# Optimization experiments

Hardware: AMD Instinct MI355X
Metric: run time of the kernel (lower is better)

Reference implementation:

```python
import jax, jax.numpy as jnp
import numpy as np
from functools import partial

B, S, H = 1, 2048, 1024
F, E, K = 2048, 8, 2


def setup_inputs() -> dict:
    key = jax.random.key(0)
    ks = jax.random.split(key, 7)
    x = jax.random.normal(ks[0], (B, S, H), dtype=jnp.float32)
    weights = jax.random.uniform(ks[1], (B * S, E), dtype=jnp.float32)
    top_weights = jax.random.uniform(ks[2], (B * S, K), dtype=jnp.float32)
    top_experts = jax.random.randint(ks[3], (B * S, K), 0, E).astype(jnp.int64)
    scale = 0.02  # keep activations in a sane range
    w1 = jax.random.normal(ks[4], (E, F, H), dtype=jnp.float32) * scale
    v1 = jax.random.normal(ks[5], (E, F, H), dtype=jnp.float32) * scale
    w2 = jax.random.normal(ks[6], (E, F, H), dtype=jnp.float32) * scale
    return {"x": x, "weights": weights, "top_weights": top_weights,
            "top_experts": top_experts, "w1": w1, "v1": v1, "w2": w2}


def _moe_forward(x, top_weights, top_experts, w1, v1, w2):
    b, s, h = x.shape
    xf = x.reshape(-1, h)  # [T, H]
    n_exp = w1.shape[0]
    # combine weight per (token, expert): sum over top-k slots routed to e
    onehot = jax.nn.one_hot(top_experts, n_exp, dtype=x.dtype)      # [T, K, E]
    cw = jnp.einsum('tk,tke->et', top_weights, onehot)              # [E, T]

    def body(acc, inputs):
        w1e, v1e, w2e, cwe = inputs  # [F,H], [F,H], [F,H], [T]
        gate = jax.nn.silu(xf @ w1e.T)       # [T, F]
        inter = gate * (xf @ v1e.T)          # GLU
        down = inter @ w2e                   # [T, H]
        return acc + cwe[:, None] * down, None

    out, _ = jax.lax.scan(body, jnp.zeros_like(xf), (w1, v1, w2, cw))
    return out.reshape(b, s, h)


def reference(x, weights, top_weights, top_experts, w1, v1, w2):
    # `weights` (full router probs) is accepted but unused, as in the original.
    return _moe_forward(x, top_weights, top_experts, w1, v1, w2)
```

## Files before the change

### kernel.cpp

```cpp
#include <hip/hip_runtime.h>
#include <hip/hip_bf16.h>


#define T_ 2048
#define H_ 1024
#define F_ 2048
#define E_ 8

#define SCAP 768
#define NSLOT (E_ * SCAP)
#define MAXT2 (NSLOT / 128)

typedef unsigned short u16;
typedef short s8v __attribute__((ext_vector_type(8)));
typedef float f4v __attribute__((ext_vector_type(4)));
typedef unsigned short u16x4 __attribute__((ext_vector_type(4)));

__device__ __forceinline__ u16 f2bf(float f) {
    union { float f; unsigned u; } v; v.f = f;
    unsigned r = v.u + 0x7FFF + ((v.u >> 16) & 1);
    return (u16)(r >> 16);
}
__device__ __forceinline__ unsigned pkbf(float a, float b) {
    __hip_bfloat162 h = __float22bfloat162_rn(make_float2(a, b));
    union { __hip_bfloat162 h; unsigned u; } c; c.h = h; return c.u;
}
__device__ __forceinline__ int4 cvt8(const float4 a, const float4 b) {
    int4 r; r.x = (int)pkbf(a.x, a.y); r.y = (int)pkbf(a.z, a.w);
    r.z = (int)pkbf(b.x, b.y); r.w = (int)pkbf(b.z, b.w); return r;
}
__device__ __forceinline__ void async16(void* lds, const void* g) {
    __builtin_amdgcn_global_load_lds(
        (const __attribute__((address_space(1))) unsigned*)g,
        (__attribute__((address_space(3))) unsigned*)lds, 16, 0, 0);
}

__global__ void router_kernel(const int* __restrict__ te, const float* __restrict__ tw,
                              int* __restrict__ slot_tok, float* __restrict__ slot_w,
                              int* __restrict__ tok_slot,
                              int* __restrict__ tile_e, int* __restrict__ tile_s,
                              int* __restrict__ ntiles) {
    __shared__ int cnt[E_];
    __shared__ int s_any;
    int tid = threadIdx.x;
    if (tid < E_) cnt[tid] = 0;
    if (tid == 0) s_any = 0;
    __syncthreads();
    int any = 0;
    for (int i = tid; i < 2 * T_; i += 256) if (i & 1) any |= te[i];
    if (any) atomicOr(&s_any, 1);
    __syncthreads();
    bool is32 = (s_any != 0);
    for (int t = tid; t < T_; t += 256) {
        int e0 = is32 ? te[2 * t]     : te[4 * t];
        int e1 = is32 ? te[2 * t + 1] : te[4 * t + 2];
        float w0 = tw[2 * t], w1 = tw[2 * t + 1];
        if (e0 == e1) {
            int p = atomicAdd(&cnt[e0], 1);
            int s = (p < SCAP) ? e0 * SCAP + p : -1;
            if (s >= 0) { slot_tok[s] = t; slot_w[s] = w0 + w1; }
            tok_slot[2 * t] = s; tok_slot[2 * t + 1] = -1;
        } else {
            int p = atomicAdd(&cnt[e0], 1);
            int s = (p < SCAP) ? e0 * SCAP + p : -1;
            if (s >= 0) { slot_tok[s] = t; slot_w[s] = w0; }
            tok_slot[2 * t] = s;
            p = atomicAdd(&cnt[e1], 1);
            s = (p < SCAP) ? e1 * SCAP + p : -1;
            if (s >= 0) { slot_tok[s] = t; slot_w[s] = w1; }
            tok_slot[2 * t + 1] = s;
        }
    }
    __syncthreads();
    for (int e = 0; e < E_; ++e) {
        int c = min(cnt[e], SCAP);
        int pc = min((c + 127) & ~127, SCAP);
        for (int p = c + tid; p < pc; p += 256) {
            slot_tok[e * SCAP + p] = -1; slot_w[e * SCAP + p] = 0.f;
        }
    }
    __syncthreads();
    if (tid == 0) {
        int nt = 0;
        for (int e = 0; e < E_; ++e) {
            int pc = min((min(cnt[e], SCAP) + 127) & ~127, SCAP);
            for (int s = 0; s < pc; s += 128) { tile_e[nt] = e; tile_s[nt] = e * SCAP + s; ++nt; }
        }
        *ntiles = nt;
    }
}

__global__ void tcvt8_kernel(const float* __restrict__ src0, u16* __restrict__ dst0) {
    const float* src = src0 + (size_t)blockIdx.z * F_ * H_;
    u16* dst = dst0 + (size_t)blockIdx.z * H_ * F_;
    __shared__ __align__(16) u16 tile[64][72];
    int bc = blockIdx.x * 64, br = blockIdx.y * 64;
    int tx = threadIdx.x, ty = threadIdx.y;
    for (int r = ty; r < 64; r += 32) {
        const float* p = src + (size_t)(br + r) * H_ + bc + tx * 8;
        float4 v0 = *(const float4*)p;
        float4 v1 = *(const float4*)(p + 4);
        u16* q = &tile[r][tx * 8];
        q[0] = f2bf(v0.x); q[1] = f2bf(v0.y); q[2] = f2bf(v0.z); q[3] = f2bf(v0.w);
        q[4] = f2bf(v1.x); q[5] = f2bf(v1.y); q[6] = f2bf(v1.z); q[7] = f2bf(v1.w);
    }
    __syncthreads();
    for (int c = ty; c < 64; c += 32) {
        u16 tmp[8];
#pragma unroll
        for (int j = 0; j < 8; ++j) tmp[j] = tile[tx * 8 + j][c];
        *(int4*)&dst[(size_t)(bc + c) * F_ + br + tx * 8] = *(int4*)tmp;
    }
}

__global__ void gather_x_kernel(const float* __restrict__ x, const int* __restrict__ slot_tok,
                                const int* __restrict__ tile_s, const int* __restrict__ ntiles,
                                u16* __restrict__ xg) {
    if ((int)blockIdx.x >= *ntiles) return;
    int base = tile_s[blockIdx.x];
    int tid = threadIdx.x;
    __shared__ int stok[128];
    if (tid < 128) stok[tid] = slot_tok[base + tid];
    __syncthreads();
    int c0 = blockIdx.y * 2048;
    for (int c = c0 + tid; c < c0 + 2048; c += 256) {
        int r = c >> 7, co = (c & 127) * 8;
        int tok = stok[r];
        u16* dst = xg + ((size_t)(base + r) << 10) + co;
        if (tok < 0) { *(int4*)dst = make_int4(0, 0, 0, 0); }
        else {
            const float* p = x + ((size_t)tok << 10) + co;
            *(int4*)dst = cvt8(*(const float4*)p, *(const float4*)(p + 4));
        }
    }
}

__global__ __launch_bounds__(256, 4) void glu_async_kernel(
        const u16* __restrict__ xg, const float* __restrict__ w1,
        const float* __restrict__ v1, const int* __restrict__ tile_e,
        const int* __restrict__ tile_s, const int* __restrict__ ntiles,
        const float* __restrict__ slot_w, u16* __restrict__ inter) {
    int bt = blockIdx.y;
    if (bt >= *ntiles) return;
    int e = tile_e[bt], s0 = tile_s[bt];
    int f0 = blockIdx.x * 64;
    __shared__ __align__(16) u16 As[2][128 * 32];
    __shared__ __align__(16) u16 B1s[2][64 * 32];
    __shared__ __align__(16) u16 B2s[2][64 * 32];
    __shared__ float swv[128];
    int tid = threadIdx.x;
    int lane = tid & 63, wave = tid >> 6;
    int wm = wave >> 1, wn = wave & 1;
    int ml = lane & 15, q = lane >> 4;
    if (tid < 128) swv[tid] = slot_w[s0 + tid];

    int row0 = (wave << 4) + (lane >> 2);
    int row1 = row0 + 64;
    int cs = ((lane & 3) ^ ((row0 >> 1) & 3)) << 3;
    const u16* gA0  = xg + ((size_t)(s0 + row0) << 10) + cs;
    const u16* gA1  = xg + ((size_t)(s0 + row1) << 10) + cs;
    int l0 = (row0 << 5) + ((lane & 3) << 3);
    int l1 = (row1 << 5) + ((lane & 3) << 3);

    int brow = tid >> 2;
    int bc   = tid & 3;
    const size_t wofs = (size_t)e * F_ * H_;
    const float* gB1 = w1 + wofs + (size_t)(f0 + brow) * H_ + bc * 8;
    const float* gB2 = v1 + wofs + (size_t)(f0 + brow) * H_ + bc * 8;
    int lb = (brow << 5) + ((bc ^ ((brow >> 1) & 3)) << 3);

    int xs = (q ^ ((lane >> 1) & 3)) << 3;

    f4v accg[4][2] = {};
    f4v accu[4][2] = {};

    float4 rb1a = *(const float4*)(gB1);
    float4 rb1b = *(const float4*)(gB1 + 4);
    float4 rb2a = *(const float4*)(gB2);
    float4 rb2b = *(const float4*)(gB2 + 4);
    async16(&As[0][l0], gA0);
    async16(&As[0][l1], gA1);

    const int NT = H_ / 32;
    int cur = 0;
    for (int t = 0; t < NT; ++t) {
        *(int4*)(&B1s[cur][lb]) = cvt8(rb1a, rb1b);
        *(int4*)(&B2s[cur][lb]) = cvt8(rb2a, rb2b);
        __syncthreads();
        if (t + 1 < NT) {
            int k = (t + 1) << 5;
            rb1a = *(const float4*)(gB1 + k);
            rb1b = *(const float4*)(gB1 + k + 4);
            rb2a = *(const float4*)(gB2 + k);
            rb2b = *(const float4*)(gB2 + k + 4);
            int nx = cur ^ 1;
            async16(&As[nx][l0], gA0 + k);
            async16(&As[nx][l1], gA1 + k);
        }
        s8v a[4], b1[2], b2[2];
#pragma unroll
        for (int i = 0; i < 4; ++i)
            a[i]  = *(const s8v*)(&As[cur][(wm * 64 + i * 16 + ml) * 32 + xs]);
#pragma unroll
        for (int j = 0; j < 2; ++j) {
            b1[j] = *(const s8v*)(&B1s[cur][(wn * 32 + j * 16 + ml) * 32 + xs]);
            b2[j] = *(const s8v*)(&B2s[cur][(wn * 32 + j * 16 + ml) * 32 + xs]);
        }
#pragma unroll
        for (int i = 0; i < 4; ++i)
#pragma unroll
            for (int j = 0; j < 2; ++j) {
                accg[i][j] = __builtin_amdgcn_mfma_f32_16x16x32_bf16(a[i], b1[j], accg[i][j], 0, 0, 0);
                accu[i][j] = __builtin_amdgcn_mfma_f32_16x16x32_bf16(a[i], b2[j], accu[i][j], 0, 0, 0);
            }
        cur ^= 1;
    }
#pragma unroll
    for (int i = 0; i < 4; ++i)
#pragma unroll
        for (int r = 0; r < 4; ++r) {
            int lr = wm * 64 + i * 16 + q * 4 + r;
            float cv = swv[lr];
#pragma unroll
            for (int j = 0; j < 2; ++j) {
                float g = accg[i][j][r];
                float u = accu[i][j][r];
                float s = g / (1.f + __expf(-g));
                int f = f0 + wn * 32 + j * 16 + ml;
                inter[((size_t)(s0 + lr) << 11) + f] = f2bf(cv * s * u);
            }
        }
}

__global__ __launch_bounds__(256, 4) void down_async_kernel(
        const u16* __restrict__ inter, const u16* __restrict__ w2bT,
        const int* __restrict__ tile_e, const int* __restrict__ tile_s,
        const int* __restrict__ ntiles,
        float* __restrict__ dbufA, float* __restrict__ dbufB) {
    int bt = blockIdx.y;
    if (bt >= *ntiles) return;
    int e = tile_e[bt], s0 = tile_s[bt];
    int h0 = blockIdx.x * 64;
    int ks = blockIdx.z;
    int kbeg = ks * (F_ / 2);
    float* dbuf = ks ? dbufB : dbufA;
    __shared__ __align__(16) u16 As[2][128 * 32];
    __shared__ __align__(16) u16 Bs[2][64 * 32];
    int tid = threadIdx.x;
    int lane = tid & 63, wave = tid >> 6;
    int wm = wave >> 1, wn = wave & 1;
    int ml = lane & 15, q = lane >> 4;

    int row0 = (wave << 4) + (lane >> 2);
    int row1 = row0 + 64;
    int cs = ((lane & 3) ^ ((row0 >> 1) & 3)) << 3;
    const u16* gA0 = inter + ((size_t)(s0 + row0) << 11) + kbeg + cs;
    const u16* gA1 = inter + ((size_t)(s0 + row1) << 11) + kbeg + cs;
    const u16* gB  = w2bT + (size_t)e * H_ * F_ + ((size_t)(h0 + row0) << 11) + kbeg + cs;
    int l0 = (row0 << 5) + ((lane & 3) << 3);
    int l1 = (row1 << 5) + ((lane & 3) << 3);
    int xs = (q ^ ((lane >> 1) & 3)) << 3;

    f4v acc[4][2] = {};

    async16(&As[0][l0], gA0);
    async16(&As[0][l1], gA1);
    async16(&Bs[0][l0], gB);

    int cur = 0;
    for (int k0 = 0; k0 < F_ / 2; k0 += 32) {
        __syncthreads();
        if (k0 + 32 < F_ / 2) {
            int nx = cur ^ 1;
            async16(&As[nx][l0], gA0 + k0 + 32);
            async16(&As[nx][l1], gA1 + k0 + 32);
            async16(&Bs[nx][l0], gB  + k0 + 32);
        }
        s8v a[4], b[2];
#pragma unroll
        for (int i = 0; i < 4; ++i)
            a[i] = *(const s8v*)(&As[cur][(wm * 64 + i * 16 + ml) * 32 + xs]);
#pragma unroll
        for (int j = 0; j < 2; ++j)
            b[j] = *(const s8v*)(&Bs[cur][(wn * 32 + j * 16 + ml) * 32 + xs]);
#pragma unroll
        for (int i = 0; i < 4; ++i)
#pragma unroll
            for (int j = 0; j < 2; ++j)
                acc[i][j] = __builtin_amdgcn_mfma_f32_16x16x32_bf16(a[i], b[j], acc[i][j], 0, 0, 0);
        cur ^= 1;
    }
#pragma unroll
    for (int i = 0; i < 4; ++i)
#pragma unroll
        for (int r = 0; r < 4; ++r) {
            int lr = wm * 64 + i * 16 + q * 4 + r;
            float* drow = dbuf + ((size_t)(s0 + lr) << 10);
#pragma unroll
            for (int j = 0; j < 2; ++j) {
                int h = h0 + wn * 32 + j * 16 + ml;
                drow[h] = acc[i][j][r];
            }
        }
}

__global__ void combine_kernel(const float* __restrict__ dbufA, const float* __restrict__ dbufB,
                               const int* __restrict__ tok_slot, float* __restrict__ out) {
    int t = blockIdx.x;
    int c = threadIdx.x * 4;
    int s0 = tok_slot[2 * t], s1 = tok_slot[2 * t + 1];
    float4 acc = make_float4(0.f, 0.f, 0.f, 0.f);
    if (s0 >= 0) {
        float4 a = *(const float4*)(dbufA + ((size_t)s0 << 10) + c);
        float4 b = *(const float4*)(dbufB + ((size_t)s0 << 10) + c);
        acc.x = a.x + b.x; acc.y = a.y + b.y; acc.z = a.z + b.z; acc.w = a.w + b.w;
    }
    if (s1 >= 0) {
        float4 a = *(const float4*)(dbufA + ((size_t)s1 << 10) + c);
        float4 b = *(const float4*)(dbufB + ((size_t)s1 << 10) + c);
        acc.x += a.x + b.x; acc.y += a.y + b.y; acc.z += a.z + b.z; acc.w += a.w + b.w;
    }
    *(float4*)(out + ((size_t)t << 10) + c) = acc;
}

#define SCAP3 1024
__global__ void router3_kernel(const int* __restrict__ te, const float* __restrict__ tw,
                               int* __restrict__ cnt_g, int* __restrict__ slot_tok,
                               float* __restrict__ slot_w) {
    __shared__ int cnt[E_];
    __shared__ int s_any;
    int tid = threadIdx.x;
    if (tid < E_) cnt[tid] = 0;
    if (tid == 0) s_any = 0;
    __syncthreads();
    int any = 0;
    for (int i = tid; i < 2 * T_; i += 256) if (i & 1) any |= te[i];
    if (any) atomicOr(&s_any, 1);
    __syncthreads();
    bool is32 = (s_any != 0);
    for (int t = tid; t < T_; t += 256) {
        int e0 = is32 ? te[2 * t]     : te[4 * t];
        int e1 = is32 ? te[2 * t + 1] : te[4 * t + 2];
        float w0 = tw[2 * t], w1 = tw[2 * t + 1];
        if (e0 == e1) {
            int p = atomicAdd(&cnt[e0], 1);
            if (p < SCAP3) { slot_tok[e0 * SCAP3 + p] = t; slot_w[e0 * SCAP3 + p] = w0 + w1; }
        } else {
            int p = atomicAdd(&cnt[e0], 1);
            if (p < SCAP3) { slot_tok[e0 * SCAP3 + p] = t; slot_w[e0 * SCAP3 + p] = w0; }
            p = atomicAdd(&cnt[e1], 1);
            if (p < SCAP3) { slot_tok[e1 * SCAP3 + p] = t; slot_w[e1 * SCAP3 + p] = w1; }
        }
    }
    __syncthreads();
    for (int e = 0; e < E_; ++e) {
        int c = min(cnt[e], SCAP3);
        int pc = min((c + 127) & ~127, SCAP3);
        for (int p = c + tid; p < pc; p += 256) {
            slot_tok[e * SCAP3 + p] = 0; slot_w[e * SCAP3 + p] = 0.f;
        }
    }
    if (tid < E_) cnt_g[tid] = min(cnt[tid], SCAP3);
}
__global__ void cvt_kernel(const float* __restrict__ src, u16* __restrict__ dst) {
    int i = (blockIdx.x * 256 + threadIdx.x) * 4;
    float4 v = *(const float4*)(src + i);
    u16x4 o = { f2bf(v.x), f2bf(v.y), f2bf(v.z), f2bf(v.w) };
    *(u16x4*)(dst + i) = o;
}
__global__ __launch_bounds__(256, 2) void glu3_kernel(
        const u16* __restrict__ xb, const float* __restrict__ w1,
        const float* __restrict__ v1, const int* __restrict__ cnt_g,
        const int* __restrict__ slot_tok, const float* __restrict__ slot_w,
        u16* __restrict__ inter) {
    int e = blockIdx.x >> 3, tt = blockIdx.x & 7;
    if (tt * 128 >= cnt_g[e]) return;
    __shared__ __align__(16) u16 As[128 * 32];
    __shared__ __align__(16) u16 B1s[128 * 32];
    __shared__ __align__(16) u16 B2s[128 * 32];
    __shared__ int stok[128];
    __shared__ float sw[128];
    int tid = threadIdx.x;
    if (tid < 128) {
        stok[tid] = slot_tok[e * SCAP3 + tt * 128 + tid];
        sw[tid]   = slot_w[e * SCAP3 + tt * 128 + tid];
    }
    __syncthreads();
    int lane = tid & 63, wave = tid >> 6;
    int wm = wave >> 1, wn = wave & 1;
    int f0 = blockIdx.y * 128;
    int ml = lane & 15, q = lane >> 4;
    int r0 = tid >> 2, r1 = 64 + (tid >> 2);
    int colo = (tid & 3) * 8;
    const size_t tokoff0 = (size_t)stok[r0] * H_ + colo;
    const size_t tokoff1 = (size_t)stok[r1] * H_ + colo;
    const float* gb1 = w1 + (size_t)e * F_ * H_ + (size_t)f0 * H_;
    const float* gb2 = v1 + (size_t)e * F_ * H_ + (size_t)f0 * H_;
    const size_t boff0 = (size_t)r0 * H_ + colo;
    const size_t boff1 = (size_t)r1 * H_ + colo;
    f4v accg[4][4] = {};
    f4v accu[4][4] = {};
    for (int k0 = 0; k0 < H_; k0 += 32) {
        __syncthreads();
        *(int4*)(As + tid * 8)         = *(const int4*)(xb + tokoff0 + k0);
        *(int4*)(As + (256 + tid) * 8) = *(const int4*)(xb + tokoff1 + k0);
        const float* p = gb1 + boff0 + k0;
        *(int4*)(B1s + tid * 8) = cvt8(*(const float4*)p, *(const float4*)(p + 4));
        p = gb1 + boff1 + k0;
        *(int4*)(B1s + (256 + tid) * 8) = cvt8(*(const float4*)p, *(const float4*)(p + 4));
        p = gb2 + boff0 + k0;
        *(int4*)(B2s + tid * 8) = cvt8(*(const float4*)p, *(const float4*)(p + 4));
        p = gb2 + boff1 + k0;
        *(int4*)(B2s + (256 + tid) * 8) = cvt8(*(const float4*)p, *(const float4*)(p + 4));
        __syncthreads();
        s8v a[4], b1[4], b2[4];
#pragma unroll
        for (int i = 0; i < 4; ++i) {
            a[i]  = *(const s8v*)(As  + (wm * 64 + i * 16 + ml) * 32 + q * 8);
            b1[i] = *(const s8v*)(B1s + (wn * 64 + i * 16 + ml) * 32 + q * 8);
            b2[i] = *(const s8v*)(B2s + (wn * 64 + i * 16 + ml) * 32 + q * 8);
        }
#pragma unroll
        for (int i = 0; i < 4; ++i)
#pragma unroll
            for (int j = 0; j < 4; ++j) {
                accg[i][j] = __builtin_amdgcn_mfma_f32_16x16x32_bf16(a[i], b1[j], accg[i][j], 0, 0, 0);
                accu[i][j] = __builtin_amdgcn_mfma_f32_16x16x32_bf16(a[i], b2[j], accu[i][j], 0, 0, 0);
            }
    }
#pragma unroll
    for (int i = 0; i < 4; ++i)
#pragma unroll
        for (int r = 0; r < 4; ++r) {
            int lr = wm * 64 + i * 16 + q * 4 + r;
            float cv = sw[lr];
#pragma unroll
            for (int j = 0; j < 4; ++j) {
                float g = accg[i][j][r];
                float u = accu[i][j][r];
                float s = g / (1.f + __expf(-g));
                int f = f0 + wn * 64 + j * 16 + ml;
                inter[(size_t)(e * SCAP3 + tt * 128 + lr) * F_ + f] = f2bf(cv * s * u);
            }
        }
}
__global__ __launch_bounds__(256) void down3_kernel(
        const u16* __restrict__ inter, const u16* __restrict__ w2bT,
        const int* __restrict__ cnt_g, const int* __restrict__ slot_tok,
        float* __restrict__ out) {
    int e = blockIdx.x >> 3, tt = blockIdx.x & 7;
    if (tt * 128 >= cnt_g[e]) return;
    __shared__ __align__(16) u16 As[128 * 32];
    __shared__ __align__(16) u16 Bs[128 * 32];
    __shared__ int stok[128];
    int tid = threadIdx.x;
    if (tid < 128) stok[tid] = slot_tok[e * SCAP3 + tt * 128 + tid];
    __syncthreads();
    int lane = tid & 63, wave = tid >> 6;
    int wm = wave >> 1, wn = wave & 1;
    int h0 = blockIdx.y * 128;
    int ml = lane & 15, q = lane >> 4;
    int kbeg = blockIdx.z * (F_ / 2), kend = kbeg + (F_ / 2);
    f4v acc[4][4] = {};
    const u16* ga = inter + (size_t)(e * SCAP3 + tt * 128) * F_;
    const u16* gb = w2bT + (size_t)e * H_ * F_ + (size_t)h0 * F_;
    for (int k0 = kbeg; k0 < kend; k0 += 32) {
        __syncthreads();
#pragma unroll
        for (int p = 0; p < 2; ++p) {
            int c = p * 256 + tid;
            int r = c >> 2, co = (c & 3) * 8;
            *(int4*)(As + c * 8) = *(const int4*)(ga + (size_t)r * F_ + k0 + co);
            *(int4*)(Bs + c * 8) = *(const int4*)(gb + (size_t)r * F_ + k0 + co);
        }
        __syncthreads();
        s8v a[4], b[4];
#pragma unroll
        for (int i = 0; i < 4; ++i) {
            a[i] = *(const s8v*)(As + (wm * 64 + i * 16 + ml) * 32 + q * 8);
            b[i] = *(const s8v*)(Bs + (wn * 64 + i * 16 + ml) * 32 + q * 8);
        }
#pragma unroll
        for (int i = 0; i < 4; ++i)
#pragma unroll
            for (int j = 0; j < 4; ++j)
                acc[i][j] = __builtin_amdgcn_mfma_f32_16x16x32_bf16(a[i], b[j], acc[i][j], 0, 0, 0);
    }
#pragma unroll
    for (int i = 0; i < 4; ++i)
#pragma unroll
        for (int r = 0; r < 4; ++r) {
            int lr = wm * 64 + i * 16 + q * 4 + r;
            size_t trow = (size_t)stok[lr] * H_;
#pragma unroll
            for (int j = 0; j < 4; ++j) {
                int h = h0 + wn * 64 + j * 16 + ml;
                atomicAdd(&out[trow + h], acc[i][j][r]);
            }
        }
}

extern "C" void kernel_launch(void* const* d_in, const int* in_sizes, int n_in,
                              void* d_out, int out_size, void* d_ws, size_t ws_size,
                              hipStream_t stream) {
    const float* x  = (const float*)d_in[0];
    const float* tw = (const float*)d_in[2];
    const int*   te = (const int*)d_in[3];
    const float* w1 = (const float*)d_in[4];
    const float* v1 = (const float*)d_in[5];
    const float* w2 = (const float*)d_in[6];
    float* out = (float*)d_out;
    char* ws = (char*)d_ws;

    if (ws_size >= ((size_t)135 << 20)) {
        int*   ntiles   = (int*)(ws);
        int*   tile_e   = (int*)(ws + 256);
        int*   tile_s   = (int*)(ws + 512);
        int*   tok_slot = (int*)(ws + (4 << 10));
        int*   slot_tok = (int*)(ws + (20 << 10));
        float* slot_w   = (float*)(ws + (44 << 10));
        u16*   xg       = (u16*)(ws + ((size_t)1 << 20));
        u16*   w2bT     = (u16*)(ws + ((size_t)77 << 20));
        u16*   inter    = (u16*)(ws + ((size_t)109 << 20));
        float* dbufA    = (float*)(ws + ((size_t)13 << 20));
        float* dbufB    = (float*)(ws + ((size_t)45 << 20));

        router_kernel<<<1, 256, 0, stream>>>(te, tw, slot_tok, slot_w, tok_slot,
                                             tile_e, tile_s, ntiles);
        tcvt8_kernel<<<dim3(H_ / 64, F_ / 64, E_), dim3(8, 32), 0, stream>>>(w2, w2bT);
        gather_x_kernel<<<dim3(MAXT2, 8), 256, 0, stream>>>(x, slot_tok, tile_s, ntiles, xg);
        glu_async_kernel<<<dim3(F_ / 64, MAXT2), 256, 0, stream>>>(
            xg, w1, v1, tile_e, tile_s, ntiles, slot_w, inter);
        down_async_kernel<<<dim3(H_ / 64, MAXT2, 2), 256, 0, stream>>>(
            inter, w2bT, tile_e, tile_s, ntiles, dbufA, dbufB);
        combine_kernel<<<T_, 256, 0, stream>>>(dbufA, dbufB, tok_slot, out);
    } else {
        int*   cnt_g    = (int*)(ws);
        int*   slot_tok = (int*)(ws + (4 << 10));
        float* slot_w   = (float*)(ws + (64 << 10));
        u16*   xb       = (u16*)(ws + ((size_t)1 << 20));
        u16*   w2bT     = (u16*)(ws + ((size_t)5 << 20));
        u16*   inter    = (u16*)(ws + ((size_t)37 << 20));

        hipMemsetAsync(out, 0, (size_t)T_ * H_ * sizeof(float), stream);
        router3_kernel<<<1, 256, 0, stream>>>(te, tw, cnt_g, slot_tok, slot_w);
        cvt_kernel<<<(T_ * H_) / 1024, 256, 0, stream>>>(x, xb);
        tcvt8_kernel<<<dim3(H_ / 64, F_ / 64, E_), dim3(8, 32), 0, stream>>>(w2, w2bT);
        glu3_kernel<<<dim3(E_ * 8, F_ / 128), 256, 0, stream>>>(
            xb, w1, v1, cnt_g, slot_tok, slot_w, inter);
        down3_kernel<<<dim3(E_ * 8, H_ / 128, 2), 256, 0, stream>>>(
            inter, w2bT, cnt_g, slot_tok, out);
    }
}
```

Measured before the change: 324.1 us.

## Deepen GLU kernel prefetch to two tiles with manual vmcnt waits and sched barriers

Unrolls the gate/up GEMM K-loop by two and keeps two sets of fp32 weight registers in flight, so the global loads for tile t+2 and t+3 are issued while earlier tiles compute. It replaces __syncthreads with explicit s_waitcnt vmcnt and s_barrier, and pins instruction order with sched_barrier so loads are not reordered past the MFMAs. This aims to hide global memory latency for the B-operand conversion path. In exchange it uses more VGPRs and relies on hand-counted vmcnt values that are brittle, and the pinned ordering may block the compiler's interleaving.

```diff
diff --git a/kernel.cpp b/kernel.cpp
--- a/kernel.cpp
+++ b/kernel.cpp
@@ -34,6 +34,7 @@
         (const __attribute__((address_space(1))) unsigned*)g,
         (__attribute__((address_space(3))) unsigned*)lds, 16, 0, 0);
 }
+#define SCHED_PIN() __builtin_amdgcn_sched_barrier(0)
 
 __global__ void router_kernel(const int* __restrict__ te, const float* __restrict__ tw,
                               int* __restrict__ slot_tok, float* __restrict__ slot_w,
@@ -174,47 +175,89 @@
     f4v accg[4][2] = {};
     f4v accu[4][2] = {};
 
-    float4 rb1a = *(const float4*)(gB1);
-    float4 rb1b = *(const float4*)(gB1 + 4);
-    float4 rb2a = *(const float4*)(gB2);
-    float4 rb2b = *(const float4*)(gB2 + 4);
+#define GLU_COMPUTE(B) do {                                                   \
+        s8v a[4], b1[2], b2[2];                                               \
+        _Pragma("unroll")                                                     \
+        for (int i = 0; i < 4; ++i)                                           \
+            a[i]  = *(const s8v*)(&As[B][(wm * 64 + i * 16 + ml) * 32 + xs]); \
+        _Pragma("unroll")                                                     \
+        for (int j = 0; j < 2; ++j) {                                         \
+            b1[j] = *(const s8v*)(&B1s[B][(wn * 32 + j * 16 + ml) * 32 + xs]);\
+            b2[j] = *(const s8v*)(&B2s[B][(wn * 32 + j * 16 + ml) * 32 + xs]);\
+        }                                                                     \
+        _Pragma("unroll")                                                     \
+        for (int i = 0; i < 4; ++i)                                           \
+            _Pragma("unroll")                                                 \
+            for (int j = 0; j < 2; ++j) {                                     \
+                accg[i][j] = __builtin_amdgcn_mfma_f32_16x16x32_bf16(         \
+                                 a[i], b1[j], accg[i][j], 0, 0, 0);           \
+                accu[i][j] = __builtin_amdgcn_mfma_f32_16x16x32_bf16(         \
+                                 a[i], b2[j], accu[i][j], 0, 0, 0);           \
+            }                                                                 \
+    } while (0)
+
+    float4 e0 = *(const float4*)(gB1);
+    float4 e1 = *(const float4*)(gB1 + 4);
+    float4 e2 = *(const float4*)(gB2);
+    float4 e3 = *(const float4*)(gB2 + 4);
+    SCHED_PIN();
     async16(&As[0][l0], gA0);
     async16(&As[0][l1], gA1);
+    SCHED_PIN();
+    float4 o0 = *(const float4*)(gB1 + 32);
+    float4 o1 = *(const float4*)(gB1 + 36);
+    float4 o2 = *(const float4*)(gB2 + 32);
+    float4 o3 = *(const float4*)(gB2 + 36);
+    SCHED_PIN();
 
     const int NT = H_ / 32;
-    int cur = 0;
-    for (int t = 0; t < NT; ++t) {
-        *(int4*)(&B1s[cur][lb]) = cvt8(rb1a, rb1b);
-        *(int4*)(&B2s[cur][lb]) = cvt8(rb2a, rb2b);
-        __syncthreads();
-        if (t + 1 < NT) {
-            int k = (t + 1) << 5;
-            rb1a = *(const float4*)(gB1 + k);
-            rb1b = *(const float4*)(gB1 + k + 4);
-            rb2a = *(const float4*)(gB2 + k);
-            rb2b = *(const float4*)(gB2 + k + 4);
-            int nx = cur ^ 1;
-            async16(&As[nx][l0], gA0 + k);
-            async16(&As[nx][l1], gA1 + k);
-        }
-        s8v a[4], b1[2], b2[2];
-#pragma unroll
-        for (int i = 0; i < 4; ++i)
-            a[i]  = *(const s8v*)(&As[cur][(wm * 64 + i * 16 + ml) * 32 + xs]);
-#pragma unroll
-        for (int j = 0; j < 2; ++j) {
-            b1[j] = *(const s8v*)(&B1s[cur][(wn * 32 + j * 16 + ml) * 32 + xs]);
-            b2[j] = *(const s8v*)(&B2s[cur][(wn * 32 + j * 16 + ml) * 32 + xs]);
-        }
-#pragma unroll
-        for (int i = 0; i < 4; ++i)
-#pragma unroll
-            for (int j = 0; j < 2; ++j) {
-                accg[i][j] = __builtin_amdgcn_mfma_f32_16x16x32_bf16(a[i], b1[j], accg[i][j], 0, 0, 0);
-                accu[i][j] = __builtin_amdgcn_mfma_f32_16x16x32_bf16(a[i], b2[j], accu[i][j], 0, 0, 0);
-            }
-        cur ^= 1;
-    }
+    for (int t = 0; t < NT; t += 2) {
+        asm volatile("s_waitcnt vmcnt(6)" ::: "memory");
+        SCHED_PIN();
+        *(int4*)(&B1s[0][lb]) = cvt8(e0, e1);
+        *(int4*)(&B2s[0][lb]) = cvt8(e2, e3);
+        SCHED_PIN();
+        asm volatile("s_waitcnt vmcnt(4) lgkmcnt(0)" ::: "memory");
+        SCHED_PIN();
+        __builtin_amdgcn_s_barrier();
+        SCHED_PIN();
+        async16(&As[1][l0], gA0 + ((t + 1) << 5));
+        async16(&As[1][l1], gA1 + ((t + 1) << 5));
+        SCHED_PIN();
+        if (t + 2 < NT) {
+            int k = (t + 2) << 5;
+            e0 = *(const float4*)(gB1 + k);
+            e1 = *(const float4*)(gB1 + k + 4);
+            e2 = *(const float4*)(gB2 + k);
+            e3 = *(const float4*)(gB2 + k + 4);
+        }
+        SCHED_PIN();
+        GLU_COMPUTE(0);
+        if (t + 2 < NT) asm volatile("s_waitcnt vmcnt(6)" ::: "memory");
+        else            asm volatile("s_waitcnt vmcnt(2)" ::: "memory");
+        SCHED_PIN();
+        *(int4*)(&B1s[1][lb]) = cvt8(o0, o1);
+        *(int4*)(&B2s[1][lb]) = cvt8(o2, o3);
+        SCHED_PIN();
+        if (t + 2 < NT) asm volatile("s_waitcnt vmcnt(4) lgkmcnt(0)" ::: "memory");
+        else            asm volatile("s_waitcnt vmcnt(0) lgkmcnt(0)" ::: "memory");
+        SCHED_PIN();
+        __builtin_amdgcn_s_barrier();
+        SCHED_PIN();
+        if (t + 2 < NT) {
+            async16(&As[0][l0], gA0 + ((t + 2) << 5));
+            async16(&As[0][l1], gA1 + ((t + 2) << 5));
+            SCHED_PIN();
+            int k = (t + 3) << 5;
+            o0 = *(const float4*)(gB1 + k);
+            o1 = *(const float4*)(gB1 + k + 4);
+            o2 = *(const float4*)(gB2 + k);
+            o3 = *(const float4*)(gB2 + k + 4);
+        }
+        SCHED_PIN();
+        GLU_COMPUTE(1);
+    }
+#undef GLU_COMPUTE
 #pragma unroll
     for (int i = 0; i < 4; ++i)
 #pragma unroll
```

After: 399.7 us. 1.23x slower.
